# Optimization experiments

Measured on AMD Instinct MI355X. Metric: run time of the kernel, lower is better.

The kernel has to match this reference:

```python
import jax, jax.numpy as jnp
import numpy as np

TEMPERATURE = 0.5
B, D = 4096, 256

def setup_inputs() -> dict:
    key = jax.random.key(0)
    k1, k2 = jax.random.split(key)
    z_i = jax.random.normal(k1, (B, D), dtype=jnp.float32)
    z_j = jax.random.normal(k2, (B, D), dtype=jnp.float32)
    return {"z_i": z_i, "z_j": z_j}

def reference(z_i, z_j):
    # NT-Xent loss (SimCLR). Cosine similarity of L2-normalized rows == dot product.
    b = z_i.shape[0]
    n = 2 * b
    zi = z_i / jnp.linalg.norm(z_i, axis=1, keepdims=True)
    zj = z_j / jnp.linalg.norm(z_j, axis=1, keepdims=True)
    z = jnp.concatenate([zi, zj], axis=0)            # [N, D]
    sim = jnp.matmul(z, z.T)                          # [N, N] cosine-sim matrix
    # positives: sim(i, i+b) and sim(i+b, i)
    pos = jnp.concatenate([jnp.diagonal(sim, offset=b), jnp.diagonal(sim, offset=-b)])  # [N]
    logits = sim / TEMPERATURE
    # Cross-entropy with the positive as the target class over {pos} U negatives.
    # The candidate set per row is all j != i (the positive j = partner(i) is included,
    # only the self-similarity diagonal is excluded) -> mask diagonal with -inf.
    neg_inf = jnp.asarray(-jnp.inf, dtype=logits.dtype)
    masked = jnp.where(jnp.eye(n, dtype=bool), neg_inf, logits)
    lse = jax.nn.logsumexp(masked, axis=1)            # [N]
    loss = jnp.sum(lse - pos / TEMPERATURE) / n
    return loss
```

## Files before the change

kernel.cpp:

```cpp
#include <hip/hip_runtime.h>
#include <hip/hip_bf16.h>


constexpr int BB = 4096;
constexpr int NN = 8192;
constexpr int DD = 256;
constexpr int TS = 128;
constexpr int NT = NN / TS;
constexpr int NBLK = NT * (NT + 1) / 2;
constexpr int KCH = 32;
constexpr int NCH = DD / KCH;

typedef _Float16 half4v __attribute__((ext_vector_type(4)));
typedef _Float16 half8v __attribute__((ext_vector_type(8)));
typedef float floatx16 __attribute__((ext_vector_type(16)));

__global__ __launch_bounds__(256) void nt_normalize(
    const float* __restrict__ zi, const float* __restrict__ zj,
    _Float16* __restrict__ Z, float* __restrict__ posPartial,
    float* __restrict__ rowsum)
{
    const int lane = threadIdx.x & 63;
    const int wave = threadIdx.x >> 6;
    const int i = blockIdx.x * 4 + wave;

    if (blockIdx.x < 32) rowsum[blockIdx.x * 256 + threadIdx.x] = 0.f;

    const float4 a = ((const float4*)(zi + (size_t)i * DD))[lane];
    const float4 b = ((const float4*)(zj + (size_t)i * DD))[lane];

    float ssi = a.x*a.x + a.y*a.y + a.z*a.z + a.w*a.w;
    float ssj = b.x*b.x + b.y*b.y + b.z*b.z + b.w*b.w;
    float dd  = a.x*b.x + a.y*b.y + a.z*b.z + a.w*b.w;
#pragma unroll
    for (int off = 32; off > 0; off >>= 1) {
        ssi += __shfl_xor(ssi, off);
        ssj += __shfl_xor(ssj, off);
        dd  += __shfl_xor(dd,  off);
    }
    const float invi = rsqrtf(ssi);
    const float invj = rsqrtf(ssj);

    half4v ha, hb;
    ha.x = (_Float16)(a.x * invi); ha.y = (_Float16)(a.y * invi);
    ha.z = (_Float16)(a.z * invi); ha.w = (_Float16)(a.w * invi);
    hb.x = (_Float16)(b.x * invj); hb.y = (_Float16)(b.y * invj);
    hb.z = (_Float16)(b.z * invj); hb.w = (_Float16)(b.w * invj);

    ((half4v*)(Z + (size_t)i * DD))[lane]        = ha;
    ((half4v*)(Z + (size_t)(BB + i) * DD))[lane] = hb;

    __shared__ float ps[4];
    if (lane == 0) ps[wave] = dd * invi * invj;
    __syncthreads();
    if (threadIdx.x == 0)
        posPartial[blockIdx.x] = ps[0] + ps[1] + ps[2] + ps[3];
}

__device__ __forceinline__ float half_sums(float x) {
    int t;
    t = __builtin_amdgcn_update_dpp(0, __builtin_bit_cast(int, x), 0x111, 0xf, 0xf, false);
    x += __builtin_bit_cast(float, t);
    t = __builtin_amdgcn_update_dpp(0, __builtin_bit_cast(int, x), 0x112, 0xf, 0xf, false);
    x += __builtin_bit_cast(float, t);
    t = __builtin_amdgcn_update_dpp(0, __builtin_bit_cast(int, x), 0x114, 0xf, 0xf, false);
    x += __builtin_bit_cast(float, t);
    t = __builtin_amdgcn_update_dpp(0, __builtin_bit_cast(int, x), 0x118, 0xf, 0xf, false);
    x += __builtin_bit_cast(float, t);
    t = __builtin_amdgcn_update_dpp(0, __builtin_bit_cast(int, x), 0x142, 0xa, 0xf, false);
    x += __builtin_bit_cast(float, t);
    return x;
}

__global__ __launch_bounds__(256, 4) void nt_simexp(
    const _Float16* __restrict__ Z, float* __restrict__ rowsum)
{
    __shared__ _Float16 sAB[2][2][TS * KCH];
    __shared__ float colacc[TS];

    const int bid = (blockIdx.x & 7) * (NBLK / 8) + (blockIdx.x >> 3);

    const int t = NBLK - 1 - bid;
    int m = (int)((sqrtf((float)(8 * t + 1)) - 1.0f) * 0.5f);
    while ((m + 1) * (m + 2) / 2 <= t) ++m;
    while (m * (m + 1) / 2 > t) --m;
    const int rt = NT - 1 - m;
    const int ct = NT - 1 - (t - m * (m + 1) / 2);
    const bool diag = (rt == ct);

    const int tid = threadIdx.x;
    const int wave = tid >> 6;
    const int lane = tid & 63;
    const int lm = lane & 31;
    const int lh = lane >> 5;
    const int wr = wave >> 1;
    const int wc = wave & 1;

    const int rbase = rt * TS;
    const int cbase = ct * TS;

    if (tid < TS) colacc[tid] = 0.f;

    const int st_row = lane >> 2;
    const int st_sg  = (lane & 3) ^ ((lane >> 3) & 3);
    const _Float16* Ap = Z + (size_t)rbase * DD;
    const _Float16* Bp = Z + (size_t)cbase * DD;

    auto stage = [&](int buf, int ch) {
#pragma unroll
        for (int j = 0; j < 2; ++j) {
            const int c = wave + 4 * j;
            const int r = 16 * c + st_row;
            const _Float16* gA = Ap + (size_t)r * DD + ch * KCH + st_sg * 8;
            __builtin_amdgcn_global_load_lds(
                (const __attribute__((address_space(1))) unsigned int*)gA,
                (__attribute__((address_space(3))) unsigned int*)(&sAB[buf][0][c * 512]),
                16, 0, 0);
            const _Float16* gB = Bp + (size_t)r * DD + ch * KCH + st_sg * 8;
            __builtin_amdgcn_global_load_lds(
                (const __attribute__((address_space(1))) unsigned int*)gB,
                (__attribute__((address_space(3))) unsigned int*)(&sAB[buf][1][c * 512]),
                16, 0, 0);
        }
    };

    floatx16 a00, a01, a10, a11;
#pragma unroll
    for (int r = 0; r < 16; ++r) { a00[r] = 0.f; a01[r] = 0.f; a10[r] = 0.f; a11[r] = 0.f; }

    stage(0, 0);

    for (int ch = 0; ch < NCH; ++ch) {
        __syncthreads();
        if (ch + 1 < NCH) stage((ch + 1) & 1, ch + 1);

        const int b = ch & 1;
        __builtin_amdgcn_s_setprio(1);
#pragma unroll
        for (int s = 0; s < 2; ++s) {
            const int pg  = 2 * s + lh;
            const int ph8 = (pg ^ ((lm >> 1) & 3)) * 8;
            half8v fa0 = *(const half8v*)&sAB[b][0][(wr * 64 +      lm) * KCH + ph8];
            half8v fa1 = *(const half8v*)&sAB[b][0][(wr * 64 + 32 + lm) * KCH + ph8];
            half8v fb0 = *(const half8v*)&sAB[b][1][(wc * 64 +      lm) * KCH + ph8];
            half8v fb1 = *(const half8v*)&sAB[b][1][(wc * 64 + 32 + lm) * KCH + ph8];
            a00 = __builtin_amdgcn_mfma_f32_32x32x16_f16(fa0, fb0, a00, 0, 0, 0);
            a01 = __builtin_amdgcn_mfma_f32_32x32x16_f16(fa0, fb1, a01, 0, 0, 0);
            a10 = __builtin_amdgcn_mfma_f32_32x32x16_f16(fa1, fb0, a10, 0, 0, 0);
            a11 = __builtin_amdgcn_mfma_f32_32x32x16_f16(fa1, fb1, a11, 0, 0, 0);
        }
        __builtin_amdgcn_s_setprio(0);
    }

    const float KEXP = 2.0f * 1.44269504088896340736f;
    float eb0 = 0.f, eb1 = 0.f;
#pragma unroll
    for (int tr = 0; tr < 2; ++tr) {
#pragma unroll
        for (int r = 0; r < 16; ++r) {
            const int mrow = (r & 3) + 8 * (r >> 2) + 4 * lh;
            float e0 = __builtin_amdgcn_exp2f((tr ? a10[r] : a00[r]) * KEXP);
            float e1 = __builtin_amdgcn_exp2f((tr ? a11[r] : a01[r]) * KEXP);
            if (diag && (wr == wc) && (mrow == lm)) {
                if (tr == 0) e0 = 0.f; else e1 = 0.f;
            }
            eb0 += e0; eb1 += e1;
            if (!diag) {
                float s2 = half_sums(e0 + e1);
                if (lm == 31)
                    atomicAdd(&colacc[wr * 64 + tr * 32 + mrow], s2);
            }
        }
    }

    eb0 += __shfl_xor(eb0, 32);
    eb1 += __shfl_xor(eb1, 32);
    if (lane < 32) {
        atomicAdd(&rowsum[cbase + wc * 64 + lm], eb0);
        atomicAdd(&rowsum[cbase + wc * 64 + 32 + lm], eb1);
    }
    if (!diag) {
        __syncthreads();
        if (tid < TS) atomicAdd(&rowsum[rbase + tid], colacc[tid]);
    }
}

__global__ __launch_bounds__(256) void nt_finalize(
    const float* __restrict__ rowsum, const float* __restrict__ posPartial,
    float* __restrict__ out)
{
    const int tid = threadIdx.x;
    float acc = 0.f;
#pragma unroll
    for (int it = 0; it < NN / 256; ++it)
        acc += __builtin_amdgcn_logf(rowsum[tid + it * 256]);
    float pacc = 0.f;
#pragma unroll
    for (int it = 0; it < 4; ++it)
        pacc += posPartial[tid + it * 256];

#pragma unroll
    for (int off = 32; off > 0; off >>= 1) {
        acc  += __shfl_xor(acc,  off);
        pacc += __shfl_xor(pacc, off);
    }
    __shared__ float sa[4], sp[4];
    const int wave = tid >> 6;
    if ((tid & 63) == 0) { sa[wave] = acc; sp[wave] = pacc; }
    __syncthreads();
    if (tid == 0) {
        const float lntot = (sa[0] + sa[1] + sa[2] + sa[3]) * 0.6931471805599453f;
        const float ptot  = sp[0] + sp[1] + sp[2] + sp[3];
        out[0] = (lntot - 4.0f * ptot) * (1.0f / (float)NN);
    }
}

extern "C" void kernel_launch(void* const* d_in, const int* in_sizes, int n_in,
                              void* d_out, int out_size, void* d_ws, size_t ws_size,
                              hipStream_t stream) {
    const float* zi = (const float*)d_in[0];
    const float* zj = (const float*)d_in[1];
    float* out = (float*)d_out;

    _Float16* Z = (_Float16*)d_ws;
    float* rowsum = (float*)((char*)d_ws + (size_t)NN * DD * 2);
    float* posPartial = rowsum + NN;

    nt_normalize<<<BB / 4, 256, 0, stream>>>(zi, zj, Z, posPartial, rowsum);
    nt_simexp<<<NBLK, 256, 0, stream>>>((const _Float16*)Z, rowsum);
    nt_finalize<<<1, 256, 0, stream>>>(rowsum, posPartial, out);
}
```

Before: 92.41 us.

## Load MFMA operands directly from global memory instead of staging through LDS

Drops the double-buffered LDS staging (global_load_lds plus per-chunk barriers) in the similarity kernel. Each wave now reads its fp16 A/B fragments straight from global memory in a fully unrolled K loop over 16 steps. This removes the LDS traffic and the per-chunk synchronisation, but gives up data sharing between waves, so there are more redundant global/L2 reads (each row is read by two waves) and less explicit latency hiding.

```diff
diff --git a/kernel.cpp b/kernel.cpp
--- a/kernel.cpp
+++ b/kernel.cpp
@@ -8,8 +8,7 @@
 constexpr int TS = 128;
 constexpr int NT = NN / TS;
 constexpr int NBLK = NT * (NT + 1) / 2;
-constexpr int KCH = 32;
-constexpr int NCH = DD / KCH;
+constexpr int KSTEPS = DD / 16;
 
 typedef _Float16 half4v __attribute__((ext_vector_type(4)));
 typedef _Float16 half8v __attribute__((ext_vector_type(8)));
@@ -75,7 +74,6 @@
 __global__ __launch_bounds__(256, 4) void nt_simexp(
     const _Float16* __restrict__ Z, float* __restrict__ rowsum)
 {
-    __shared__ _Float16 sAB[2][2][TS * KCH];
     __shared__ float colacc[TS];
 
     const int bid = (blockIdx.x & 7) * (NBLK / 8) + (blockIdx.x >> 3);
@@ -100,56 +98,28 @@
     const int cbase = ct * TS;
 
     if (tid < TS) colacc[tid] = 0.f;
-
-    const int st_row = lane >> 2;
-    const int st_sg  = (lane & 3) ^ ((lane >> 3) & 3);
-    const _Float16* Ap = Z + (size_t)rbase * DD;
-    const _Float16* Bp = Z + (size_t)cbase * DD;
-
-    auto stage = [&](int buf, int ch) {
-#pragma unroll
-        for (int j = 0; j < 2; ++j) {
-            const int c = wave + 4 * j;
-            const int r = 16 * c + st_row;
-            const _Float16* gA = Ap + (size_t)r * DD + ch * KCH + st_sg * 8;
-            __builtin_amdgcn_global_load_lds(
-                (const __attribute__((address_space(1))) unsigned int*)gA,
-                (__attribute__((address_space(3))) unsigned int*)(&sAB[buf][0][c * 512]),
-                16, 0, 0);
-            const _Float16* gB = Bp + (size_t)r * DD + ch * KCH + st_sg * 8;
-            __builtin_amdgcn_global_load_lds(
-                (const __attribute__((address_space(1))) unsigned int*)gB,
-                (__attribute__((address_space(3))) unsigned int*)(&sAB[buf][1][c * 512]),
-                16, 0, 0);
-        }
-    };
+    __syncthreads();
+
+    const _Float16* ar0 = Z + (size_t)(rbase + wr * 64 + lm) * DD + lh * 8;
+    const _Float16* ar1 = ar0 + 32 * DD;
+    const _Float16* br0 = Z + (size_t)(cbase + wc * 64 + lm) * DD + lh * 8;
+    const _Float16* br1 = br0 + 32 * DD;
 
     floatx16 a00, a01, a10, a11;
 #pragma unroll
     for (int r = 0; r < 16; ++r) { a00[r] = 0.f; a01[r] = 0.f; a10[r] = 0.f; a11[r] = 0.f; }
 
-    stage(0, 0);
-
-    for (int ch = 0; ch < NCH; ++ch) {
-        __syncthreads();
-        if (ch + 1 < NCH) stage((ch + 1) & 1, ch + 1);
-
-        const int b = ch & 1;
-        __builtin_amdgcn_s_setprio(1);
-#pragma unroll
-        for (int s = 0; s < 2; ++s) {
-            const int pg  = 2 * s + lh;
-            const int ph8 = (pg ^ ((lm >> 1) & 3)) * 8;
-            half8v fa0 = *(const half8v*)&sAB[b][0][(wr * 64 +      lm) * KCH + ph8];
-            half8v fa1 = *(const half8v*)&sAB[b][0][(wr * 64 + 32 + lm) * KCH + ph8];
-            half8v fb0 = *(const half8v*)&sAB[b][1][(wc * 64 +      lm) * KCH + ph8];
-            half8v fb1 = *(const half8v*)&sAB[b][1][(wc * 64 + 32 + lm) * KCH + ph8];
-            a00 = __builtin_amdgcn_mfma_f32_32x32x16_f16(fa0, fb0, a00, 0, 0, 0);
-            a01 = __builtin_amdgcn_mfma_f32_32x32x16_f16(fa0, fb1, a01, 0, 0, 0);
-            a10 = __builtin_amdgcn_mfma_f32_32x32x16_f16(fa1, fb0, a10, 0, 0, 0);
-            a11 = __builtin_amdgcn_mfma_f32_32x32x16_f16(fa1, fb1, a11, 0, 0, 0);
-        }
-        __builtin_amdgcn_s_setprio(0);
+#pragma unroll
+    for (int ks = 0; ks < KSTEPS; ++ks) {
+        const int off = ks * 16;
+        half8v fa0 = *(const half8v*)(ar0 + off);
+        half8v fa1 = *(const half8v*)(ar1 + off);
+        half8v fb0 = *(const half8v*)(br0 + off);
+        half8v fb1 = *(const half8v*)(br1 + off);
+        a00 = __builtin_amdgcn_mfma_f32_32x32x16_f16(fa0, fb0, a00, 0, 0, 0);
+        a01 = __builtin_amdgcn_mfma_f32_32x32x16_f16(fa0, fb1, a01, 0, 0, 0);
+        a10 = __builtin_amdgcn_mfma_f32_32x32x16_f16(fa1, fb0, a10, 0, 0, 0);
+        a11 = __builtin_amdgcn_mfma_f32_32x32x16_f16(fa1, fb1, a11, 0, 0, 0);
     }
 
     const float KEXP = 2.0f * 1.44269504088896340736f;
```

Measured after the change: 131.4 us. 42.1% more time.
